# Performance work log

Hardware: AMD Instinct MI355X
Metric: run time of the kernel (lower is better)

The kernel has to match this reference:

```python
import jax, jax.numpy as jnp
import numpy as np

# Faithful JAX port of RayObsGraph.forward with T=1.
# torch_geometric GraphConv(x, edge_index) with add-aggregation and no edge
# weights computes: out[i] = lin_root(x[i]) + lin_rel(sum_{(j->i) in E} x[j]),
# where lin_root has no bias and lin_rel has a bias. dense_to_sparse(adj)
# yields an edge (row j -> col i) for every nonzero adj[j, i], so the
# aggregation equals binarize(adj)^T @ x, computed batched here instead of the
# original per-sample Python loop.

GS = 128      # graph_size
OBS = 1024    # obs_dim
H = 256       # gcn_h_size
OUT = 1024    # gcn_outsize
NO = 18       # num_outputs
B = 256

def setup_inputs() -> dict:
    key = jax.random.key(0)
    ks = jax.random.split(key, 16)
    inp = {
        "flat": jax.random.normal(ks[0], (B, OBS), jnp.float32),
        "nodes": jax.random.normal(ks[1], (B, GS, OBS), jnp.float32),
        "num_nodes": jax.random.randint(ks[2], (B,), 0, GS),
        "adj": jax.random.randint(ks[3], (B, GS, GS), 0, 2),
        "seq_lens": jnp.ones((B,), jnp.int32),
        # GraphConv 0: lin_rel (bias) + lin_root (no bias)
        "W0_rel": jax.random.normal(ks[4], (OBS, H), jnp.float32) / np.sqrt(OBS),
        "b0": jnp.zeros((H,), jnp.float32),
        "W0_root": jax.random.normal(ks[5], (OBS, H), jnp.float32) / np.sqrt(OBS),
        # GraphConv 1
        "W1_rel": jax.random.normal(ks[6], (H, OUT), jnp.float32) / np.sqrt(H),
        "b1": jnp.zeros((OUT,), jnp.float32),
        "W1_root": jax.random.normal(ks[7], (H, OUT), jnp.float32) / np.sqrt(H),
        # logit / value branches (SlimFC, activation None)
        "Wl": jax.random.normal(ks[8], (OUT, NO), jnp.float32) / np.sqrt(OUT),
        "bl": jnp.zeros((NO,), jnp.float32),
        "Wv": jax.random.normal(ks[9], (OUT, 1), jnp.float32) / np.sqrt(OUT),
        "bv": jnp.zeros((1,), jnp.float32),
    }
    return inp

def _forward(flat, nodes, adj, num_nodes,
             W0_rel, b0, W0_root, W1_rel, b1, W1_root, Wl, bl, Wv, bv):
    bsz = flat.shape[0]
    bi = jnp.arange(bsz)
    n = num_nodes
    nm1 = jnp.maximum(n - 1, 0)
    has_prev = n > 0

    # dense_to_sparse treats any nonzero entry as an edge (weight unused)
    A = (adj != 0).astype(flat.dtype)                       # [B, GS, GS]
    A = A.at[bi, n, n].set(1.0)
    A = A.at[bi, n, nm1].set(jnp.where(has_prev, 1.0, A[bi, n, nm1]))
    A = A.at[bi, nm1, n].set(jnp.where(has_prev, 1.0, A[bi, nm1, n]))

    # write current observation into node slot num_nodes
    x = nodes.at[bi, n].set(flat)                           # [B, GS, OBS]

    At = jnp.swapaxes(A, 1, 2)                              # message j->i: A^T
    aggr0 = jnp.einsum('bij,bjd->bid', At, x)               # [B, GS, OBS]
    h0 = jax.nn.relu(aggr0 @ W0_rel + b0 + x @ W0_root)     # [B, GS, H]
    aggr1 = jnp.einsum('bij,bjd->bid', At, h0)              # [B, GS, H]
    h1 = jax.nn.relu(aggr1 @ W1_rel + b1 + h0 @ W1_root)    # [B, GS, OUT]

    node_out = h1[bi, n]                                    # [B, OUT]
    logits = node_out @ Wl + bl                             # [B, NO]
    values = (node_out @ Wv + bv).squeeze(-1)               # [B]
    return logits, values

def reference(flat, nodes, num_nodes, adj, seq_lens,
              W0_rel, b0, W0_root, W1_rel, b1, W1_root, Wl, bl, Wv, bv):
    # seq_lens only determines B = len(seq_lens); T = flat.shape[0] // B = 1
    del seq_lens
    return _forward(flat, nodes, adj, num_nodes,
                    W0_rel, b0, W0_root, W1_rel, b1, W1_root, Wl, bl, Wv, bv)
```

## Files before the change

kernel.cpp:

```cpp
#include <hip/hip_runtime.h>
#include <hip/hip_bf16.h>
#include <cstdint>
#include <cstddef>

#define GS     128
#define OBS    1024
#define HSZ    256
#define OUTSZ  1024
#define NOUT   18
#define BATCH  256

typedef short  short8  __attribute__((ext_vector_type(8)));
typedef float  f32x4   __attribute__((ext_vector_type(4)));

__device__ __forceinline__ uint32_t f2bf_bits(float f) {
  uint32_t u = __builtin_bit_cast(uint32_t, f);
  return (u + 0x7fffu + ((u >> 16) & 1u)) >> 16;
}
__device__ __forceinline__ float bf_bits2f(uint32_t b) {
  return __builtin_bit_cast(float, b << 16);
}
__device__ __forceinline__ uint4 cvt8s(const float4 a, const float4 b) {
  float v[8] = {a.x, a.y, a.z, a.w, b.x, b.y, b.z, b.w};
  uint32_t h[8];
#pragma unroll
  for (int e = 0; e < 8; ++e) h[e] = f2bf_bits(v[e]);
  return make_uint4(h[0] | (h[1] << 16), h[2] | (h[3] << 16),
                    h[4] | (h[5] << 16), h[6] | (h[7] << 16));
}

__device__ __forceinline__ void bar_lds() {
  asm volatile("s_waitcnt lgkmcnt(0)" ::: "memory");
  __builtin_amdgcn_s_barrier();
  __builtin_amdgcn_sched_barrier(0);
}

__global__ __launch_bounds__(256) void prep_kernel(
    const float* __restrict__ W0_rel, const float* __restrict__ W0_root,
    ushort* __restrict__ WtP, const float* __restrict__ Wl,
    const float* __restrict__ Wv, float* __restrict__ WlT,
    const float* __restrict__ W1_rel, const float* __restrict__ W1_root,
    ushort* __restrict__ W1bf)
{
  __shared__ float T[64][65];
  const int blk = blockIdx.x;
  const int t = threadIdx.x;
  if (blk < 128) {
    const int k0 = (blk & 15) * 64;
    const int n0 = (blk >> 4) * 64;
    for (int idx = t; idx < 4096; idx += 256) {
      const int r = idx >> 6, c = idx & 63;
      const int n = n0 + c;
      T[r][c] = (n < HSZ) ? W0_rel[(size_t)(k0 + r) * HSZ + n]
                          : W0_root[(size_t)(k0 + r) * HSZ + (n - HSZ)];
    }
    __syncthreads();
    for (int idx = t; idx < 512; idx += 256) {
      const int nl = idx >> 3;
      const int kc = idx & 7;
      uint32_t h[8];
#pragma unroll
      for (int e = 0; e < 8; ++e) h[e] = f2bf_bits(T[kc * 8 + e][nl]);
      const int kg = k0 + kc * 8;
      const uint4 w = make_uint4(h[0] | (h[1] << 16), h[2] | (h[3] << 16),
                                 h[4] | (h[5] << 16), h[6] | (h[7] << 16));
      *(uint4*)&WtP[((size_t)((kg >> 5) * 512 + n0 + nl)) * 32 + (kg & 31)] = w;
    }
  } else if (blk < 132) {
    const int o = (blk - 128) * 256 + t;
#pragma unroll
    for (int c = 0; c < NOUT; ++c)
      WlT[(size_t)c * OUTSZ + o] = Wl[(size_t)o * NOUT + c];
    WlT[(size_t)18 * OUTSZ + o] = Wv[o];
  } else {
    const int base = (blk - 132) * 16384;
    for (int it = 0; it < 64; ++it) {
      const int idx = base + it * 256 + t;
      const int k = idx >> 10, o = idx & 1023;
      const float v = (k < HSZ) ? W1_rel[(size_t)k * OUTSZ + o]
                                : W1_root[(size_t)(k - HSZ) * OUTSZ + o];
      W1bf[idx] = (ushort)f2bf_bits(v);
    }
  }
}

__global__ __launch_bounds__(512, 2) void mega_kernel(
    const float* __restrict__ flat, const float* __restrict__ nodes,
    const int* __restrict__ num_nodes, const int* __restrict__ adj,
    const float* __restrict__ b0, const ushort* __restrict__ WtP,
    const ushort* __restrict__ W1bf, const float* __restrict__ b1,
    const float* __restrict__ WlT, const float* __restrict__ bl,
    const float* __restrict__ bv, float* __restrict__ out)
{
  __shared__ alignas(16) char smem[135168];
  ushort (*Ys)[264]     = (ushort (*)[264])smem;
  ushort (*As)[128][40] = (ushort (*)[128][40])smem;
  float  (*part)[4]     = (float  (*)[4])smem;
  __shared__ uint32_t rm[128][4];
  __shared__ uint32_t cmL[128][4];
  __shared__ float    a1s[256];
  __shared__ float    rns[256];
  __shared__ float    pl[19][4];

  const int b  = blockIdx.x;
  const int nb = num_nodes[b];
  const int t  = threadIdx.x;
  const int wv = t >> 6, lane = t & 63;
  const int ln = lane & 15, q = lane >> 4;

#pragma unroll 4
  for (int i = 0; i < 16; ++i) {
    const int k = wv * 16 + i;
    const int* arow = adj + ((size_t)b * GS + k) * GS;
    const unsigned long long m0 = __ballot(arow[lane] != 0);
    const unsigned long long m1 = __ballot(arow[64 + lane] != 0);
    if (lane == 0) {
      rm[k][0] = (uint32_t)m0; rm[k][1] = (uint32_t)(m0 >> 32);
      rm[k][2] = (uint32_t)m1; rm[k][3] = (uint32_t)(m1 >> 32);
    }
  }
  __syncthreads();
  if (t < 128) {
    uint32_t c0 = 0, c1 = 0, c2 = 0, c3 = 0;
    const int w = t >> 5, sh = t & 31;
#pragma unroll 8
    for (int k = 0; k < 128; ++k) {
      const uint32_t bit = (rm[k][w] >> sh) & 1u;
      if (k < 32)      c0 |= bit << k;
      else if (k < 64) c1 |= bit << (k - 32);
      else if (k < 96) c2 |= bit << (k - 64);
      else             c3 |= bit << (k - 96);
    }
    cmL[t][0] = c0; cmL[t][1] = c1; cmL[t][2] = c2; cmL[t][3] = c3;
  }
  __syncthreads();
  if (t == 0) {
    cmL[nb][nb >> 5] |= 1u << (nb & 31);
    if (nb > 0) {
      cmL[nb - 1][nb >> 5] |= 1u << (nb & 31);
      cmL[nb][(nb - 1) >> 5] |= 1u << ((nb - 1) & 31);
    }
  }

  const int arow2 = t >> 2;
  const int akb   = (t & 3) * 8;
  const float* xsrc = ((arow2 == nb) ? (flat + (size_t)b * OBS)
                                     : (nodes + ((size_t)b * GS + arow2) * OBS)) + akb;
  const ushort* bptr = WtP + ((size_t)(wv * 64 + ln)) * 32 + q * 8;

  f32x4 acc[4][8] = {};

  {
    const float4 c0 = *(const float4*)(xsrc);
    const float4 c1 = *(const float4*)(xsrc + 4);
    *(uint4*)&As[0][arow2][akb] = cvt8s(c0, c1);
  }
  short8 bc0 = *(const short8*)(bptr);
  short8 bc1 = *(const short8*)(bptr + 512);
  short8 bc2 = *(const short8*)(bptr + 1024);
  short8 bc3 = *(const short8*)(bptr + 1536);
  float4 gA = *(const float4*)(xsrc + 32);
  float4 gB = *(const float4*)(xsrc + 36);
  bar_lds();

  for (int s = 0; s < 32; s += 2) {
    {
      const ushort* bp = bptr + (size_t)(s + 1) * 16384;
      const short8 bn0 = *(const short8*)(bp);
      const short8 bn1 = *(const short8*)(bp + 512);
      const short8 bn2 = *(const short8*)(bp + 1024);
      const short8 bn3 = *(const short8*)(bp + 1536);
      float4 fA = {}, fB = {};
      if (s + 2 < 32) {
        fA = *(const float4*)(xsrc + (s + 2) * 32);
        fB = *(const float4*)(xsrc + (s + 2) * 32 + 4);
      }
      short8 ah[8];
#pragma unroll
      for (int ii = 0; ii < 8; ++ii)
        ah[ii] = *(const short8*)&As[0][ii * 16 + ln][q * 8];
#pragma unroll
      for (int ii = 0; ii < 8; ++ii) {
        acc[0][ii] = __builtin_amdgcn_mfma_f32_16x16x32_bf16(bc0, ah[ii], acc[0][ii], 0, 0, 0);
        acc[1][ii] = __builtin_amdgcn_mfma_f32_16x16x32_bf16(bc1, ah[ii], acc[1][ii], 0, 0, 0);
        acc[2][ii] = __builtin_amdgcn_mfma_f32_16x16x32_bf16(bc2, ah[ii], acc[2][ii], 0, 0, 0);
        acc[3][ii] = __builtin_amdgcn_mfma_f32_16x16x32_bf16(bc3, ah[ii], acc[3][ii], 0, 0, 0);
      }
      *(uint4*)&As[1][arow2][akb] = cvt8s(gA, gB);
      gA = fA; gB = fB;
      bc0 = bn0; bc1 = bn1; bc2 = bn2; bc3 = bn3;
      bar_lds();
    }
    {
      short8 bn0 = {}, bn1 = {}, bn2 = {}, bn3 = {};
      if (s + 2 < 32) {
        const ushort* bp = bptr + (size_t)(s + 2) * 16384;
        bn0 = *(const short8*)(bp);
        bn1 = *(const short8*)(bp + 512);
        bn2 = *(const short8*)(bp + 1024);
        bn3 = *(const short8*)(bp + 1536);
      }
      float4 fA = {}, fB = {};
      if (s + 3 < 32) {
        fA = *(const float4*)(xsrc + (s + 3) * 32);
        fB = *(const float4*)(xsrc + (s + 3) * 32 + 4);
      }
      short8 ah[8];
#pragma unroll
      for (int ii = 0; ii < 8; ++ii)
        ah[ii] = *(const short8*)&As[1][ii * 16 + ln][q * 8];
#pragma unroll
      for (int ii = 0; ii < 8; ++ii) {
        acc[0][ii] = __builtin_amdgcn_mfma_f32_16x16x32_bf16(bc0, ah[ii], acc[0][ii], 0, 0, 0);
        acc[1][ii] = __builtin_amdgcn_mfma_f32_16x16x32_bf16(bc1, ah[ii], acc[1][ii], 0, 0, 0);
        acc[2][ii] = __builtin_amdgcn_mfma_f32_16x16x32_bf16(bc2, ah[ii], acc[2][ii], 0, 0, 0);
        acc[3][ii] = __builtin_amdgcn_mfma_f32_16x16x32_bf16(bc3, ah[ii], acc[3][ii], 0, 0, 0);
      }
      if (s + 2 < 32)
        *(uint4*)&As[0][arow2][akb] = cvt8s(gA, gB);
      gA = fA; gB = fB;
      bc0 = bn0; bc1 = bn1; bc2 = bn2; bc3 = bn3;
      bar_lds();
    }
  }

#pragma unroll
  for (int jj = 0; jj < 4; ++jj) {
    const int cat = wv * 64 + jj * 16 + q * 4;
    const int h   = cat & 255;
    const int kof = (cat < 256) ? 0 : 128;
#pragma unroll
    for (int ii = 0; ii < 8; ++ii) {
      const int kk = kof + ii * 16 + ln;
#pragma unroll
      for (int r = 0; r < 4; ++r)
        Ys[h + r][kk] = (ushort)f2bf_bits(acc[jj][ii][r]);
    }
  }
  __syncthreads();

  f32x4 acc2[8][2] = {};
#pragma unroll
  for (int ks = 0; ks < 4; ++ks) {
    const short8 bf0 = *(const short8*)&Ys[wv * 32 + ln][ks * 32 + q * 8];
    const short8 bf1 = *(const short8*)&Ys[wv * 32 + 16 + ln][ks * 32 + q * 8];
#pragma unroll
    for (int jt = 0; jt < 8; ++jt) {
      const uint32_t w = cmL[jt * 16 + ln][ks];
      const uint32_t byte_ = (w >> (q * 8)) & 0xFFu;
      short8 af;
#pragma unroll
      for (int i = 0; i < 8; ++i)
        af[i] = (short)(((byte_ >> i) & 1u) ? 0x3F80 : 0);
      acc2[jt][0] = __builtin_amdgcn_mfma_f32_16x16x32_bf16(af, bf0, acc2[jt][0], 0, 0, 0);
      acc2[jt][1] = __builtin_amdgcn_mfma_f32_16x16x32_bf16(af, bf1, acc2[jt][1], 0, 0, 0);
    }
  }

  const uint32_t S0 = cmL[nb][0], S1 = cmL[nb][1],
                 S2 = cmL[nb][2], S3 = cmL[nb][3];
  const float bb0 = b0[wv * 32 + ln];
  const float bb1 = b0[wv * 32 + 16 + ln];

  float asum0 = 0.f, asum1 = 0.f;
#pragma unroll
  for (int jt = 0; jt < 8; ++jt)
#pragma unroll
    for (int r = 0; r < 4; ++r) {
      const int j = jt * 16 + q * 4 + r;
      const uint32_t Sw = (j < 32) ? S0 : (j < 64) ? S1 : (j < 96) ? S2 : S3;
      const bool sj = (Sw >> (j & 31)) & 1u;
      const bool isn = (j == nb);
      {
        const int hl = wv * 32 + ln;
        const float yroot = bf_bits2f(Ys[hl][128 + j]);
        const float v = fmaxf(bb0 + yroot + acc2[jt][0][r], 0.f);
        if (sj) asum0 += v;
        if (isn) rns[hl] = v;
      }
      {
        const int hl = wv * 32 + 16 + ln;
        const float yroot = bf_bits2f(Ys[hl][128 + j]);
        const float v = fmaxf(bb1 + yroot + acc2[jt][1][r], 0.f);
        if (sj) asum1 += v;
        if (isn) rns[hl] = v;
      }
    }
  asum0 += __shfl_down(asum0, 32);
  asum0 += __shfl_down(asum0, 16);
  asum1 += __shfl_down(asum1, 32);
  asum1 += __shfl_down(asum1, 16);
  if (q == 0) {
    a1s[wv * 32 + ln]      = asum0;
    a1s[wv * 32 + 16 + ln] = asum1;
  }
  __syncthreads();

  const int oh = t >> 8;
  const int o4 = (t & 255) * 4;
  float4 a = make_float4(0.f, 0.f, 0.f, 0.f);
  if (oh == 0) a = *(const float4*)&b1[o4];
  const ushort* wp = W1bf + (size_t)oh * 256 * OUTSZ + o4;
  const float* sv = oh ? rns : a1s;
#pragma unroll 8
  for (int k = 0; k < 256; ++k) {
    const ushort4 w4 = *(const ushort4*)(wp + (size_t)k * OUTSZ);
    const float s = sv[k];
    a.x = fmaf(s, bf_bits2f(w4.x), a.x);
    a.y = fmaf(s, bf_bits2f(w4.y), a.y);
    a.z = fmaf(s, bf_bits2f(w4.z), a.z);
    a.w = fmaf(s, bf_bits2f(w4.w), a.w);
  }
  if (oh == 1) *(float4*)&part[t & 255][0] = a;
  __syncthreads();
  if (oh == 0) {
    const float4 pb = *(const float4*)&part[t & 255][0];
    a.x = fmaxf(a.x + pb.x, 0.f);
    a.y = fmaxf(a.y + pb.y, 0.f);
    a.z = fmaxf(a.z + pb.z, 0.f);
    a.w = fmaxf(a.w + pb.w, 0.f);
    float p[19];
#pragma unroll
    for (int c = 0; c < 19; ++c) {
      const float4 w = *(const float4*)&WlT[(size_t)c * OUTSZ + o4];
      p[c] = a.x * w.x + a.y * w.y + a.z * w.z + a.w * w.w;
    }
#pragma unroll
    for (int c = 0; c < 19; ++c) {
      float v = p[c];
      v += __shfl_down(v, 32); v += __shfl_down(v, 16);
      v += __shfl_down(v, 8);  v += __shfl_down(v, 4);
      v += __shfl_down(v, 2);  v += __shfl_down(v, 1);
      if (lane == 0) pl[c][wv] = v;
    }
  }
  __syncthreads();
  if (t < 19) {
    const float s = pl[t][0] + pl[t][1] + pl[t][2] + pl[t][3];
    if (t < NOUT) out[(size_t)b * NOUT + t] = s + bl[t];
    else          out[(size_t)BATCH * NOUT + b] = s + bv[0];
  }
}

extern "C" void kernel_launch(void* const* d_in, const int* in_sizes, int n_in,
                              void* d_out, int out_size, void* d_ws, size_t ws_size,
                              hipStream_t stream)
{
  const float* flat      = (const float*)d_in[0];
  const float* nodes     = (const float*)d_in[1];
  const int*   num_nodes = (const int*)  d_in[2];
  const int*   adj       = (const int*)  d_in[3];
  const float* W0_rel    = (const float*)d_in[5];
  const float* b0        = (const float*)d_in[6];
  const float* W0_root   = (const float*)d_in[7];
  const float* W1_rel    = (const float*)d_in[8];
  const float* b1        = (const float*)d_in[9];
  const float* W1_root   = (const float*)d_in[10];
  const float* Wl        = (const float*)d_in[11];
  const float* bl        = (const float*)d_in[12];
  const float* Wv        = (const float*)d_in[13];
  const float* bv        = (const float*)d_in[14];
  float* out = (float*)d_out;

  char* ws = (char*)d_ws;
  ushort* WtP  = (ushort*)ws;  ws += (size_t)512 * OBS * 2;
  float*  WlT  = (float*)ws;   ws += (size_t)19 * OUTSZ * 4;
  ushort* W1bf = (ushort*)ws;  ws += (size_t)512 * OUTSZ * 2;

  prep_kernel<<<164, 256, 0, stream>>>(
      W0_rel, W0_root, WtP, Wl, Wv, WlT, W1_rel, W1_root, W1bf);
  mega_kernel<<<BATCH, 512, 0, stream>>>(
      flat, nodes, num_nodes, adj, b0, WtP, W1bf, b1, WlT, bl, bv, out);
}
```

Before: 299.7 us.

## Double K-tile width in stage-0 GEMM and batch adjacency row loads

The first GEMM now stages 64-wide K chunks of the node features into LDS instead of 32-wide ones. This halves the number of barriers, to 16 iterations, and issues the next global loads between the two MFMA halves of each iteration to overlap latency. The adjacency bitmask build now loads all 16 rows per wave up front before the ballots, instead of interleaving loads and ballots. It raises register pressure from more in-flight loads and a larger LDS tile, which could hurt occupancy at the 512x2 launch bound.

Result: faster. 292.9 us (-2.3%).

```diff
diff --git a/kernel.cpp b/kernel.cpp
--- a/kernel.cpp
+++ b/kernel.cpp
@@ -94,7 +94,7 @@
 {
   __shared__ alignas(16) char smem[135168];
   ushort (*Ys)[264]     = (ushort (*)[264])smem;
-  ushort (*As)[128][40] = (ushort (*)[128][40])smem;
+  ushort (*As)[128][72] = (ushort (*)[128][72])smem;
   float  (*part)[4]     = (float  (*)[4])smem;
   __shared__ uint32_t rm[128][4];
   __shared__ uint32_t cmL[128][4];
@@ -108,15 +108,23 @@
   const int wv = t >> 6, lane = t & 63;
   const int ln = lane & 15, q = lane >> 4;
 
-#pragma unroll 4
-  for (int i = 0; i < 16; ++i) {
-    const int k = wv * 16 + i;
-    const int* arow = adj + ((size_t)b * GS + k) * GS;
-    const unsigned long long m0 = __ballot(arow[lane] != 0);
-    const unsigned long long m1 = __ballot(arow[64 + lane] != 0);
-    if (lane == 0) {
-      rm[k][0] = (uint32_t)m0; rm[k][1] = (uint32_t)(m0 >> 32);
-      rm[k][2] = (uint32_t)m1; rm[k][3] = (uint32_t)(m1 >> 32);
+  {
+    const int* abase = adj + ((size_t)b * GS + wv * 16) * GS;
+    int va[16], vb[16];
+#pragma unroll
+    for (int i = 0; i < 16; ++i) {
+      va[i] = abase[i * GS + lane];
+      vb[i] = abase[i * GS + 64 + lane];
+    }
+#pragma unroll
+    for (int i = 0; i < 16; ++i) {
+      const int k = wv * 16 + i;
+      const unsigned long long m0 = __ballot(va[i] != 0);
+      const unsigned long long m1 = __ballot(vb[i] != 0);
+      if (lane == 0) {
+        rm[k][0] = (uint32_t)m0; rm[k][1] = (uint32_t)(m0 >> 32);
+        rm[k][2] = (uint32_t)m1; rm[k][3] = (uint32_t)(m1 >> 32);
+      }
     }
   }
   __syncthreads();
@@ -143,7 +151,7 @@
   }
 
   const int arow2 = t >> 2;
-  const int akb   = (t & 3) * 8;
+  const int akb   = (t & 3) * 16;
   const float* xsrc = ((arow2 == nb) ? (flat + (size_t)b * OBS)
                                      : (nodes + ((size_t)b * GS + arow2) * OBS)) + akb;
   const ushort* bptr = WtP + ((size_t)(wv * 64 + ln)) * 32 + q * 8;
@@ -151,77 +159,72 @@
   f32x4 acc[4][8] = {};
 
   {
-    const float4 c0 = *(const float4*)(xsrc);
-    const float4 c1 = *(const float4*)(xsrc + 4);
-    *(uint4*)&As[0][arow2][akb] = cvt8s(c0, c1);
-  }
-  short8 bc0 = *(const short8*)(bptr);
-  short8 bc1 = *(const short8*)(bptr + 512);
-  short8 bc2 = *(const short8*)(bptr + 1024);
-  short8 bc3 = *(const short8*)(bptr + 1536);
-  float4 gA = *(const float4*)(xsrc + 32);
-  float4 gB = *(const float4*)(xsrc + 36);
+    const float4 a0 = *(const float4*)(xsrc);
+    const float4 a1 = *(const float4*)(xsrc + 4);
+    const float4 a2 = *(const float4*)(xsrc + 8);
+    const float4 a3 = *(const float4*)(xsrc + 12);
+    *(uint4*)&As[0][arow2][akb]     = cvt8s(a0, a1);
+    *(uint4*)&As[0][arow2][akb + 8] = cvt8s(a2, a3);
+  }
+  float4 g0 = *(const float4*)(xsrc + 64);
+  float4 g1 = *(const float4*)(xsrc + 68);
+  float4 g2 = *(const float4*)(xsrc + 72);
+  float4 g3 = *(const float4*)(xsrc + 76);
+  short8 bA0 = *(const short8*)(bptr);
+  short8 bA1 = *(const short8*)(bptr + 512);
+  short8 bA2 = *(const short8*)(bptr + 1024);
+  short8 bA3 = *(const short8*)(bptr + 1536);
   bar_lds();
 
-  for (int s = 0; s < 32; s += 2) {
-    {
-      const ushort* bp = bptr + (size_t)(s + 1) * 16384;
-      const short8 bn0 = *(const short8*)(bp);
-      const short8 bn1 = *(const short8*)(bp + 512);
-      const short8 bn2 = *(const short8*)(bp + 1024);
-      const short8 bn3 = *(const short8*)(bp + 1536);
-      float4 fA = {}, fB = {};
-      if (s + 2 < 32) {
-        fA = *(const float4*)(xsrc + (s + 2) * 32);
-        fB = *(const float4*)(xsrc + (s + 2) * 32 + 4);
-      }
-      short8 ah[8];
-#pragma unroll
-      for (int ii = 0; ii < 8; ++ii)
-        ah[ii] = *(const short8*)&As[0][ii * 16 + ln][q * 8];
-#pragma unroll
-      for (int ii = 0; ii < 8; ++ii) {
-        acc[0][ii] = __builtin_amdgcn_mfma_f32_16x16x32_bf16(bc0, ah[ii], acc[0][ii], 0, 0, 0);
-        acc[1][ii] = __builtin_amdgcn_mfma_f32_16x16x32_bf16(bc1, ah[ii], acc[1][ii], 0, 0, 0);
-        acc[2][ii] = __builtin_amdgcn_mfma_f32_16x16x32_bf16(bc2, ah[ii], acc[2][ii], 0, 0, 0);
-        acc[3][ii] = __builtin_amdgcn_mfma_f32_16x16x32_bf16(bc3, ah[ii], acc[3][ii], 0, 0, 0);
-      }
-      *(uint4*)&As[1][arow2][akb] = cvt8s(gA, gB);
-      gA = fA; gB = fB;
-      bc0 = bn0; bc1 = bn1; bc2 = bn2; bc3 = bn3;
-      bar_lds();
-    }
-    {
-      short8 bn0 = {}, bn1 = {}, bn2 = {}, bn3 = {};
-      if (s + 2 < 32) {
-        const ushort* bp = bptr + (size_t)(s + 2) * 16384;
-        bn0 = *(const short8*)(bp);
-        bn1 = *(const short8*)(bp + 512);
-        bn2 = *(const short8*)(bp + 1024);
-        bn3 = *(const short8*)(bp + 1536);
-      }
-      float4 fA = {}, fB = {};
-      if (s + 3 < 32) {
-        fA = *(const float4*)(xsrc + (s + 3) * 32);
-        fB = *(const float4*)(xsrc + (s + 3) * 32 + 4);
-      }
-      short8 ah[8];
-#pragma unroll
-      for (int ii = 0; ii < 8; ++ii)
-        ah[ii] = *(const short8*)&As[1][ii * 16 + ln][q * 8];
-#pragma unroll
-      for (int ii = 0; ii < 8; ++ii) {
-        acc[0][ii] = __builtin_amdgcn_mfma_f32_16x16x32_bf16(bc0, ah[ii], acc[0][ii], 0, 0, 0);
-        acc[1][ii] = __builtin_amdgcn_mfma_f32_16x16x32_bf16(bc1, ah[ii], acc[1][ii], 0, 0, 0);
-        acc[2][ii] = __builtin_amdgcn_mfma_f32_16x16x32_bf16(bc2, ah[ii], acc[2][ii], 0, 0, 0);
-        acc[3][ii] = __builtin_amdgcn_mfma_f32_16x16x32_bf16(bc3, ah[ii], acc[3][ii], 0, 0, 0);
-      }
-      if (s + 2 < 32)
-        *(uint4*)&As[0][arow2][akb] = cvt8s(gA, gB);
-      gA = fA; gB = fB;
-      bc0 = bn0; bc1 = bn1; bc2 = bn2; bc3 = bn3;
-      bar_lds();
-    }
+  for (int s = 0; s < 16; ++s) {
+    const int buf = s & 1;
+    const ushort* bpB = bptr + ((size_t)(2 * s + 1)) * 16384;
+    const short8 bB0 = *(const short8*)(bpB);
+    const short8 bB1 = *(const short8*)(bpB + 512);
+    const short8 bB2 = *(const short8*)(bpB + 1024);
+    const short8 bB3 = *(const short8*)(bpB + 1536);
+    short8 ah[8];
+#pragma unroll
+    for (int ii = 0; ii < 8; ++ii)
+      ah[ii] = *(const short8*)&As[buf][ii * 16 + ln][q * 8];
+#pragma unroll
+    for (int ii = 0; ii < 8; ++ii) {
+      acc[0][ii] = __builtin_amdgcn_mfma_f32_16x16x32_bf16(bA0, ah[ii], acc[0][ii], 0, 0, 0);
+      acc[1][ii] = __builtin_amdgcn_mfma_f32_16x16x32_bf16(bA1, ah[ii], acc[1][ii], 0, 0, 0);
+      acc[2][ii] = __builtin_amdgcn_mfma_f32_16x16x32_bf16(bA2, ah[ii], acc[2][ii], 0, 0, 0);
+      acc[3][ii] = __builtin_amdgcn_mfma_f32_16x16x32_bf16(bA3, ah[ii], acc[3][ii], 0, 0, 0);
+    }
+    short8 ah2[8];
+#pragma unroll
+    for (int ii = 0; ii < 8; ++ii)
+      ah2[ii] = *(const short8*)&As[buf][ii * 16 + ln][32 + q * 8];
+    if (s + 1 < 16) {
+      *(uint4*)&As[buf ^ 1][arow2][akb]     = cvt8s(g0, g1);
+      *(uint4*)&As[buf ^ 1][arow2][akb + 8] = cvt8s(g2, g3);
+    }
+    short8 nA0 = {}, nA1 = {}, nA2 = {}, nA3 = {};
+    if (s + 1 < 16) {
+      const ushort* bpA = bptr + ((size_t)(2 * s + 2)) * 16384;
+      nA0 = *(const short8*)(bpA);
+      nA1 = *(const short8*)(bpA + 512);
+      nA2 = *(const short8*)(bpA + 1024);
+      nA3 = *(const short8*)(bpA + 1536);
+    }
+    if (s + 2 < 16) {
+      g0 = *(const float4*)(xsrc + (s + 2) * 64);
+      g1 = *(const float4*)(xsrc + (s + 2) * 64 + 4);
+      g2 = *(const float4*)(xsrc + (s + 2) * 64 + 8);
+      g3 = *(const float4*)(xsrc + (s + 2) * 64 + 12);
+    }
+#pragma unroll
+    for (int ii = 0; ii < 8; ++ii) {
+      acc[0][ii] = __builtin_amdgcn_mfma_f32_16x16x32_bf16(bB0, ah2[ii], acc[0][ii], 0, 0, 0);
+      acc[1][ii] = __builtin_amdgcn_mfma_f32_16x16x32_bf16(bB1, ah2[ii], acc[1][ii], 0, 0, 0);
+      acc[2][ii] = __builtin_amdgcn_mfma_f32_16x16x32_bf16(bB2, ah2[ii], acc[2][ii], 0, 0, 0);
+      acc[3][ii] = __builtin_amdgcn_mfma_f32_16x16x32_bf16(bB3, ah2[ii], acc[3][ii], 0, 0, 0);
+    }
+    bA0 = nA0; bA1 = nA1; bA2 = nA2; bA3 = nA3;
+    bar_lds();
   }
 
 #pragma unroll
```
